# Performance work log

Measured on AMD Instinct MI355X. Metric: run time of the kernel, lower is better.

Reference implementation:

```python
import jax, jax.numpy as jnp
import numpy as np

D_MODEL = 1024
N_HEADS = 16
HEAD_DIM = D_MODEL // N_HEADS


def setup_inputs() -> dict:
    key = jax.random.key(0)
    ks = jax.random.split(key, 6)
    B, S = 2, 2048
    scale = 1.0 / np.sqrt(D_MODEL)
    x = jax.random.normal(ks[0], (B, S, D_MODEL), dtype=jnp.float32)
    Wq = jax.random.normal(ks[1], (D_MODEL, D_MODEL), dtype=jnp.float32) * scale
    Wk = jax.random.normal(ks[2], (D_MODEL, D_MODEL), dtype=jnp.float32) * scale
    Wv = jax.random.normal(ks[3], (D_MODEL, D_MODEL), dtype=jnp.float32) * scale
    Wo = jax.random.normal(ks[4], (D_MODEL, D_MODEL), dtype=jnp.float32) * scale
    bo = jax.random.normal(ks[5], (D_MODEL,), dtype=jnp.float32) * 0.02
    return {"x": x, "Wq": Wq, "Wk": Wk, "Wv": Wv, "Wo": Wo, "bo": bo}


def reference(x, Wq, Wk, Wv, Wo, bo):
    B, S, _ = x.shape
    H, hd = N_HEADS, HEAD_DIM
    # qkv projections (no bias, qkv_bias=False)
    q = (x @ Wq).reshape(B, S, H, hd).transpose(0, 2, 1, 3)  # [B,H,S,hd]
    k = (x @ Wk).reshape(B, S, H, hd).transpose(0, 2, 1, 3)
    v = (x @ Wv).reshape(B, S, H, hd).transpose(0, 2, 1, 3)
    scores = jnp.einsum('bhqd,bhkd->bhqk', q, k)  # [B,H,S,S]
    causal = jnp.tril(jnp.ones((S, S), dtype=bool))  # True = keep
    scores = jnp.where(causal, scores, -jnp.inf)
    weights = jax.nn.softmax(scores / np.sqrt(hd), axis=-1)
    # dropout p=0.0 -> identity
    ctx = jnp.einsum('bhqk,bhkd->bhqd', weights, v)  # [B,H,S,hd]
    ctx = ctx.transpose(0, 2, 1, 3).reshape(B, S, H * hd)
    return ctx @ Wo + bo
```

## Files before the change

kernel.cpp:

```cpp
#include <hip/hip_runtime.h>
#include <hip/hip_bf16.h>
#include <stdint.h>

#define SEQ    2048
#define BATCH  2
#define DMODEL 1024
#define NHEADS 16
#define HDIM   64
#define MROWS  (BATCH*SEQ)

typedef __attribute__((ext_vector_type(8))) short bf16x8;
typedef __attribute__((ext_vector_type(4))) float f32x4;

__device__ inline void global_to_lds16(const void* g, void* l) {
  __builtin_amdgcn_global_load_lds(
      (const __attribute__((address_space(1))) uint32_t*)g,
      (__attribute__((address_space(3))) uint32_t*)l, 16, 0, 0);
}

__device__ inline unsigned short f2bf_bits(float f) {
  __hip_bfloat16 h = __float2bfloat16(f);
  return *(unsigned short*)&h;
}

__global__ void cvt_x(const float* __restrict__ x, __hip_bfloat16* __restrict__ xb) {
  int i = (blockIdx.x * 256 + threadIdx.x) * 4;
  float4 v = *(const float4*)(x + i);
  ushort4 o;
  o.x = f2bf_bits(v.x); o.y = f2bf_bits(v.y);
  o.z = f2bf_bits(v.z); o.w = f2bf_bits(v.w);
  *(ushort4*)(xb + i) = o;
}

__global__ void trans_w(const float* __restrict__ Wq, const float* __restrict__ Wk,
                        const float* __restrict__ Wv, const float* __restrict__ Wo,
                        __hip_bfloat16* __restrict__ Wqkv_t, __hip_bfloat16* __restrict__ Wo_t) {
  __shared__ float tile[32][33];
  int z = blockIdx.z;
  const float* W = (z == 0) ? Wq : (z == 1) ? Wk : (z == 2) ? Wv : Wo;
  __hip_bfloat16* dst = (z < 3) ? (Wqkv_t + (size_t)z * 1024 * 1024) : Wo_t;
  int k0 = blockIdx.x * 32, n0 = blockIdx.y * 32;
  int tx = threadIdx.x & 31, ty = threadIdx.x >> 5;
#pragma unroll
  for (int r = 0; r < 4; r++)
    tile[ty + r * 8][tx] = W[(size_t)(k0 + ty + r * 8) * 1024 + n0 + tx];
  __syncthreads();
#pragma unroll
  for (int r = 0; r < 4; r++)
    dst[(size_t)(n0 + ty + r * 8) * 1024 + k0 + tx] = __float2bfloat16(tile[tx][ty + r * 8]);
}

__global__ void trans_v(const __hip_bfloat16* __restrict__ QKV, __hip_bfloat16* __restrict__ Vt) {
  __shared__ __hip_bfloat16 tile[64][72];
  int bh = blockIdx.y;
  int b = bh >> 4, h = bh & 15;
  int s0 = blockIdx.x * 64;
  int t = threadIdx.x;
  int r = t >> 2, cg = (t & 3) * 16;
  const __hip_bfloat16* src = QKV + ((size_t)(b * SEQ + s0 + r)) * 3072 + 2048 + h * 64 + cg;
  *(uint4*)&tile[r][cg]     = *(const uint4*)src;
  *(uint4*)&tile[r][cg + 8] = *(const uint4*)(src + 8);
  __syncthreads();
  unsigned short tmp[16];
#pragma unroll
  for (int i = 0; i < 16; i++) tmp[i] = *(const unsigned short*)&tile[cg + i][r];
  __hip_bfloat16* dst = Vt + ((size_t)bh * 64 + r) * 2048 + s0 + cg;
  *(uint4*)dst       = *(const uint4*)&tmp[0];
  *(uint4*)(dst + 8) = *(const uint4*)&tmp[8];
}

template <bool OUT_BF16>
__global__ __launch_bounds__(256, 2)
void gemm_kernel(const __hip_bfloat16* __restrict__ A, const __hip_bfloat16* __restrict__ Bt,
                 void* __restrict__ C, const float* __restrict__ bias, int ldc) {
  __shared__ __hip_bfloat16 Asl[128 * 32];
  __shared__ __hip_bfloat16 Bsl[128 * 32];

  const int t = threadIdx.x;
  const int lane = t & 63;
  const int w = t >> 6;
  const int wm = w >> 1, wn = w & 1;
  const int m0 = blockIdx.y * 128;
  const int n0 = blockIdx.x * 128;

  f32x4 acc[4][4];
#pragma unroll
  for (int i = 0; i < 4; i++)
#pragma unroll
    for (int j = 0; j < 4; j++) acc[i][j] = (f32x4){0.f, 0.f, 0.f, 0.f};

  const int rA0 = w * 16 + (lane >> 2);
  const int kof = (lane & 3) * 8;
  const int fm = lane & 15;
  const int fk = (lane >> 4) * 8;

  for (int k0 = 0; k0 < 1024; k0 += 32) {
#pragma unroll
    for (int i = 0; i < 2; i++) {
      int r = rA0 + i * 64;
      global_to_lds16(A + (size_t)(m0 + r) * 1024 + k0 + kof, (void*)(Asl + r * 32 + kof));
      global_to_lds16(Bt + (size_t)(n0 + r) * 1024 + k0 + kof, (void*)(Bsl + r * 32 + kof));
    }
    __syncthreads();
    bf16x8 af[4], bfr[4];
#pragma unroll
    for (int mi = 0; mi < 4; mi++)
      af[mi] = *(const bf16x8*)(Asl + (wm * 64 + mi * 16 + fm) * 32 + fk);
#pragma unroll
    for (int ni = 0; ni < 4; ni++)
      bfr[ni] = *(const bf16x8*)(Bsl + (wn * 64 + ni * 16 + fm) * 32 + fk);
#pragma unroll
    for (int mi = 0; mi < 4; mi++)
#pragma unroll
      for (int ni = 0; ni < 4; ni++)
        acc[mi][ni] = __builtin_amdgcn_mfma_f32_16x16x32_bf16(af[mi], bfr[ni], acc[mi][ni], 0, 0, 0);
    __syncthreads();
  }

#pragma unroll
  for (int mi = 0; mi < 4; mi++) {
    int mb = m0 + wm * 64 + mi * 16 + (lane >> 4) * 4;
#pragma unroll
    for (int ni = 0; ni < 4; ni++) {
      int n = n0 + wn * 64 + ni * 16 + fm;
      float bv = OUT_BF16 ? 0.f : bias[n];
#pragma unroll
      for (int r = 0; r < 4; r++) {
        if (OUT_BF16)
          ((__hip_bfloat16*)C)[(size_t)(mb + r) * ldc + n] = __float2bfloat16(acc[mi][ni][r]);
        else
          ((float*)C)[(size_t)(mb + r) * ldc + n] = acc[mi][ni][r] + bv;
      }
    }
  }
}

__global__ __launch_bounds__(256, 2)
void attn_kernel(const __hip_bfloat16* __restrict__ QKV,
                 const __hip_bfloat16* __restrict__ Vt,
                 __hip_bfloat16* __restrict__ ctx) {
  __shared__ __hip_bfloat16 Klds[64 * 64];
  __shared__ __hip_bfloat16 Vlds[64 * 64];
  __shared__ __hip_bfloat16 Plds[2][64 * 72];

  const int t = threadIdx.x;
  const int lane = t & 63;
  const int w = t >> 6;
  const int jb = blockIdx.x;
  const int qtab[2] = { jb, 31 - jb };
  const int bh = blockIdx.y;
  const int b = bh >> 4, h = bh & 15;
  const int fm = lane & 15;
  const int g4 = lane >> 4;
  const int fk = g4 * 8;
  const size_t rowb = (size_t)b * SEQ;
  const float c = 0.18033688011112042f;

  const int rr = lane >> 3;
  const int jc = (lane & 7) ^ rr;

  bf16x8 qf[2][2];
#pragma unroll
  for (int hh = 0; hh < 2; hh++) {
    const __hip_bfloat16* qp = QKV + (rowb + qtab[hh] * 64 + w * 16 + fm) * 3072 + h * 64 + fk;
    bf16x8 r0 = *(const bf16x8*)qp;
    bf16x8 r1 = *(const bf16x8*)(qp + 32);
#pragma unroll
    for (int i = 0; i < 8; i++) {
      float f0 = __uint_as_float(((unsigned)(unsigned short)r0[i]) << 16) * c;
      float f1 = __uint_as_float(((unsigned)(unsigned short)r1[i]) << 16) * c;
      r0[i] = (short)f2bf_bits(f0);
      r1[i] = (short)f2bf_bits(f1);
    }
    qf[hh][0] = r0; qf[hh][1] = r1;
  }

  bf16x8 ones;
#pragma unroll
  for (int i = 0; i < 8; i++) ones[i] = (short)0x3F80;

  f32x4 acc[2][4];
  f32x4 lacc[2];
#pragma unroll
  for (int hh = 0; hh < 2; hh++) {
    lacc[hh] = (f32x4){0.f, 0.f, 0.f, 0.f};
#pragma unroll
    for (int d = 0; d < 4; d++) acc[hh][d] = (f32x4){0.f, 0.f, 0.f, 0.f};
  }

  for (int ktt = 0; ktt <= qtab[1]; ++ktt) {
    const int kt0 = ktt * 64;
    __syncthreads();
#pragma unroll
    for (int i = 0; i < 2; i++) {
      int seg = w + i * 4;
      int r = seg * 8 + rr;
      global_to_lds16(QKV + (rowb + kt0 + r) * 3072 + 1024 + h * 64 + jc * 8,
                      (void*)(Klds + seg * 512 + lane * 8));
      global_to_lds16(Vt + ((size_t)bh * 64 + r) * 2048 + kt0 + jc * 8,
                      (void*)(Vlds + seg * 512 + lane * 8));
    }
    __syncthreads();

#pragma unroll
    for (int hh = 0; hh < 2; hh++) {
      if (ktt > qtab[hh]) continue;
      f32x4 s[4];
#pragma unroll
      for (int ns = 0; ns < 4; ns++) s[ns] = (f32x4){0.f, 0.f, 0.f, 0.f};
#pragma unroll
      for (int kk = 0; kk < 2; kk++) {
#pragma unroll
        for (int ns = 0; ns < 4; ns++) {
          bf16x8 kf = *(const bf16x8*)(Klds + (ns * 16 + fm) * 64 + (((kk * 4 + g4) ^ (fm & 7)) << 3));
          s[ns] = __builtin_amdgcn_mfma_f32_16x16x32_bf16(qf[hh][kk], kf, s[ns], 0, 0, 0);
        }
      }
      const bool diag = (ktt == qtab[hh]);
      __hip_bfloat16* P = (__hip_bfloat16*)Plds[hh];
#pragma unroll
      for (int ns = 0; ns < 4; ns++)
#pragma unroll
        for (int r = 0; r < 4; r++) {
          bool msk = diag && (ns * 16 + fm > w * 16 + g4 * 4 + r);
          float p = msk ? 0.f : exp2f(s[ns][r]);
          P[(w * 16 + g4 * 4 + r) * 72 + ns * 16 + fm] = __float2bfloat16(p);
        }
#pragma unroll
      for (int kk = 0; kk < 2; kk++) {
        bf16x8 pa = *(const bf16x8*)(P + (w * 16 + fm) * 72 + kk * 32 + fk);
        lacc[hh] = __builtin_amdgcn_mfma_f32_16x16x32_bf16(pa, ones, lacc[hh], 0, 0, 0);
#pragma unroll
        for (int dd = 0; dd < 4; dd++) {
          bf16x8 vf = *(const bf16x8*)(Vlds + (dd * 16 + fm) * 64 + (((kk * 4 + g4) ^ (fm & 7)) << 3));
          acc[hh][dd] = __builtin_amdgcn_mfma_f32_16x16x32_bf16(pa, vf, acc[hh][dd], 0, 0, 0);
        }
      }
    }
  }

#pragma unroll
  for (int hh = 0; hh < 2; hh++) {
#pragma unroll
    for (int dd = 0; dd < 4; dd++)
#pragma unroll
      for (int r = 0; r < 4; r++) {
        int q = qtab[hh] * 64 + w * 16 + g4 * 4 + r;
        ctx[(rowb + q) * 1024 + h * 64 + dd * 16 + fm] =
            __float2bfloat16(acc[hh][dd][r] / lacc[hh][r]);
      }
  }
}

extern "C" void kernel_launch(void* const* d_in, const int* in_sizes, int n_in,
                              void* d_out, int out_size, void* d_ws, size_t ws_size,
                              hipStream_t stream) {
  const float* x  = (const float*)d_in[0];
  const float* Wq = (const float*)d_in[1];
  const float* Wk = (const float*)d_in[2];
  const float* Wv = (const float*)d_in[3];
  const float* Wo = (const float*)d_in[4];
  const float* bo = (const float*)d_in[5];
  float* out = (float*)d_out;

  char* ws = (char*)d_ws;
  __hip_bfloat16* xb     = (__hip_bfloat16*)(ws);
  __hip_bfloat16* Wqkv_t = (__hip_bfloat16*)(ws + (8ull  << 20));
  __hip_bfloat16* Wo_t   = (__hip_bfloat16*)(ws + (14ull << 20));
  __hip_bfloat16* QKV    = (__hip_bfloat16*)(ws + (16ull << 20));
  __hip_bfloat16* ctxb   = (__hip_bfloat16*)(ws + (40ull << 20));
  __hip_bfloat16* Vt     = xb;

  cvt_x<<<dim3(MROWS * DMODEL / (256 * 4)), dim3(256), 0, stream>>>(x, xb);
  trans_w<<<dim3(32, 32, 4), dim3(256), 0, stream>>>(Wq, Wk, Wv, Wo, Wqkv_t, Wo_t);
  gemm_kernel<true><<<dim3(24, 32), dim3(256), 0, stream>>>(xb, Wqkv_t, (void*)QKV, nullptr, 3072);
  trans_v<<<dim3(32, 32), dim3(256), 0, stream>>>(QKV, Vt);
  attn_kernel<<<dim3(16, 32), dim3(256), 0, stream>>>(QKV, Vt, ctxb);
  gemm_kernel<false><<<dim3(8, 32), dim3(256), 0, stream>>>(ctxb, Wo_t, (void*)out, bo, 1024);
}
```

Measured before the change: 199.3 us.

## Stage 128-key K/V tiles in attention and retile output GEMM to 128x64

The attention kernel now loads 128 keys of K and V per barrier pair instead of 64, and processes them as two 64-wide sub-chunks. This halves the number of synchronisation and load rounds, at the cost of double the K/V LDS footprint. The V layout uses a new 16-slot XOR swizzle. The output projection GEMM switches to 128x64 tiles with each wave owning 32 rows, which doubles the grid to fill more CUs. The QKV GEMM's launch bounds now ask for 3 workgroups per CU, which may constrain registers.

```diff
diff --git a/kernel.cpp b/kernel.cpp
--- a/kernel.cpp
+++ b/kernel.cpp
@@ -69,23 +69,25 @@
   *(uint4*)(dst + 8) = *(const uint4*)&tmp[8];
 }
 
-template <bool OUT_BF16>
-__global__ __launch_bounds__(256, 2)
+template <int TN, bool OUT_BF16, int MINW>
+__global__ __launch_bounds__(256, MINW)
 void gemm_kernel(const __hip_bfloat16* __restrict__ A, const __hip_bfloat16* __restrict__ Bt,
                  void* __restrict__ C, const float* __restrict__ bias, int ldc) {
   __shared__ __hip_bfloat16 Asl[128 * 32];
-  __shared__ __hip_bfloat16 Bsl[128 * 32];
+  __shared__ __hip_bfloat16 Bsl[TN * 32];
 
   const int t = threadIdx.x;
   const int lane = t & 63;
   const int w = t >> 6;
-  const int wm = w >> 1, wn = w & 1;
+  constexpr int MI = (TN == 128) ? 4 : 2;
+  const int wrow = (TN == 128) ? (w >> 1) * 64 : w * 32;
+  const int wcol = (TN == 128) ? (w & 1) * 64 : 0;
   const int m0 = blockIdx.y * 128;
-  const int n0 = blockIdx.x * 128;
-
-  f32x4 acc[4][4];
-#pragma unroll
-  for (int i = 0; i < 4; i++)
+  const int n0 = blockIdx.x * TN;
+
+  f32x4 acc[MI][4];
+#pragma unroll
+  for (int i = 0; i < MI; i++)
 #pragma unroll
     for (int j = 0; j < 4; j++) acc[i][j] = (f32x4){0.f, 0.f, 0.f, 0.f};
 
@@ -99,18 +101,22 @@
     for (int i = 0; i < 2; i++) {
       int r = rA0 + i * 64;
       global_to_lds16(A + (size_t)(m0 + r) * 1024 + k0 + kof, (void*)(Asl + r * 32 + kof));
+    }
+#pragma unroll
+    for (int i = 0; i < TN / 64; i++) {
+      int r = rA0 + i * 64;
       global_to_lds16(Bt + (size_t)(n0 + r) * 1024 + k0 + kof, (void*)(Bsl + r * 32 + kof));
     }
     __syncthreads();
-    bf16x8 af[4], bfr[4];
-#pragma unroll
-    for (int mi = 0; mi < 4; mi++)
-      af[mi] = *(const bf16x8*)(Asl + (wm * 64 + mi * 16 + fm) * 32 + fk);
+    bf16x8 af[MI], bfr[4];
+#pragma unroll
+    for (int mi = 0; mi < MI; mi++)
+      af[mi] = *(const bf16x8*)(Asl + (wrow + mi * 16 + fm) * 32 + fk);
 #pragma unroll
     for (int ni = 0; ni < 4; ni++)
-      bfr[ni] = *(const bf16x8*)(Bsl + (wn * 64 + ni * 16 + fm) * 32 + fk);
-#pragma unroll
-    for (int mi = 0; mi < 4; mi++)
+      bfr[ni] = *(const bf16x8*)(Bsl + (wcol + ni * 16 + fm) * 32 + fk);
+#pragma unroll
+    for (int mi = 0; mi < MI; mi++)
 #pragma unroll
       for (int ni = 0; ni < 4; ni++)
         acc[mi][ni] = __builtin_amdgcn_mfma_f32_16x16x32_bf16(af[mi], bfr[ni], acc[mi][ni], 0, 0, 0);
@@ -118,11 +124,11 @@
   }
 
 #pragma unroll
-  for (int mi = 0; mi < 4; mi++) {
-    int mb = m0 + wm * 64 + mi * 16 + (lane >> 4) * 4;
+  for (int mi = 0; mi < MI; mi++) {
+    int mb = m0 + wrow + mi * 16 + (lane >> 4) * 4;
 #pragma unroll
     for (int ni = 0; ni < 4; ni++) {
-      int n = n0 + wn * 64 + ni * 16 + fm;
+      int n = n0 + wcol + ni * 16 + fm;
       float bv = OUT_BF16 ? 0.f : bias[n];
 #pragma unroll
       for (int r = 0; r < 4; r++) {
@@ -139,8 +145,8 @@
 void attn_kernel(const __hip_bfloat16* __restrict__ QKV,
                  const __hip_bfloat16* __restrict__ Vt,
                  __hip_bfloat16* __restrict__ ctx) {
-  __shared__ __hip_bfloat16 Klds[64 * 64];
-  __shared__ __hip_bfloat16 Vlds[64 * 64];
+  __shared__ __hip_bfloat16 Klds[128 * 64];
+  __shared__ __hip_bfloat16 Vlds[64 * 128];
   __shared__ __hip_bfloat16 Plds[2][64 * 72];
 
   const int t = threadIdx.x;
@@ -156,8 +162,10 @@
   const size_t rowb = (size_t)b * SEQ;
   const float c = 0.18033688011112042f;
 
-  const int rr = lane >> 3;
-  const int jc = (lane & 7) ^ rr;
+  const int krr = lane >> 3;
+  const int kjc = (lane & 7) ^ krr;
+  const int vrr = lane >> 4;
+  const int vjc = (lane & 15) ^ vrr;
 
   bf16x8 qf[2][2];
 #pragma unroll
@@ -188,52 +196,60 @@
     for (int d = 0; d < 4; d++) acc[hh][d] = (f32x4){0.f, 0.f, 0.f, 0.f};
   }
 
-  for (int ktt = 0; ktt <= qtab[1]; ++ktt) {
-    const int kt0 = ktt * 64;
-    __syncthreads();
-#pragma unroll
-    for (int i = 0; i < 2; i++) {
+  const int lastt = qtab[1] >> 1;
+  for (int ktt2 = 0; ktt2 <= lastt; ++ktt2) {
+    const int kt0 = ktt2 * 128;
+    __syncthreads();
+#pragma unroll
+    for (int i = 0; i < 4; i++) {
       int seg = w + i * 4;
-      int r = seg * 8 + rr;
-      global_to_lds16(QKV + (rowb + kt0 + r) * 3072 + 1024 + h * 64 + jc * 8,
+      int kr = seg * 8 + krr;
+      global_to_lds16(QKV + (rowb + kt0 + kr) * 3072 + 1024 + h * 64 + kjc * 8,
                       (void*)(Klds + seg * 512 + lane * 8));
-      global_to_lds16(Vt + ((size_t)bh * 64 + r) * 2048 + kt0 + jc * 8,
+      int vr = seg * 4 + vrr;
+      global_to_lds16(Vt + ((size_t)bh * 64 + vr) * 2048 + kt0 + vjc * 8,
                       (void*)(Vlds + seg * 512 + lane * 8));
     }
     __syncthreads();
 
 #pragma unroll
-    for (int hh = 0; hh < 2; hh++) {
-      if (ktt > qtab[hh]) continue;
-      f32x4 s[4];
-#pragma unroll
-      for (int ns = 0; ns < 4; ns++) s[ns] = (f32x4){0.f, 0.f, 0.f, 0.f};
-#pragma unroll
-      for (int kk = 0; kk < 2; kk++) {
-#pragma unroll
-        for (int ns = 0; ns < 4; ns++) {
-          bf16x8 kf = *(const bf16x8*)(Klds + (ns * 16 + fm) * 64 + (((kk * 4 + g4) ^ (fm & 7)) << 3));
-          s[ns] = __builtin_amdgcn_mfma_f32_16x16x32_bf16(qf[hh][kk], kf, s[ns], 0, 0, 0);
+    for (int sc = 0; sc < 2; sc++) {
+      const int kts = ktt2 * 2 + sc;
+#pragma unroll
+      for (int hh = 0; hh < 2; hh++) {
+        if (kts > qtab[hh]) continue;
+        f32x4 s[4];
+#pragma unroll
+        for (int ns = 0; ns < 4; ns++) s[ns] = (f32x4){0.f, 0.f, 0.f, 0.f};
+#pragma unroll
+        for (int kk = 0; kk < 2; kk++) {
+#pragma unroll
+          for (int ns = 0; ns < 4; ns++) {
+            int row = sc * 64 + ns * 16 + fm;
+            bf16x8 kf = *(const bf16x8*)(Klds + row * 64 + (((kk * 4 + g4) ^ (fm & 7)) << 3));
+            s[ns] = __builtin_amdgcn_mfma_f32_16x16x32_bf16(qf[hh][kk], kf, s[ns], 0, 0, 0);
+          }
         }
-      }
-      const bool diag = (ktt == qtab[hh]);
-      __hip_bfloat16* P = (__hip_bfloat16*)Plds[hh];
-#pragma unroll
-      for (int ns = 0; ns < 4; ns++)
-#pragma unroll
-        for (int r = 0; r < 4; r++) {
-          bool msk = diag && (ns * 16 + fm > w * 16 + g4 * 4 + r);
-          float p = msk ? 0.f : exp2f(s[ns][r]);
-          P[(w * 16 + g4 * 4 + r) * 72 + ns * 16 + fm] = __float2bfloat16(p);
-        }
-#pragma unroll
-      for (int kk = 0; kk < 2; kk++) {
-        bf16x8 pa = *(const bf16x8*)(P + (w * 16 + fm) * 72 + kk * 32 + fk);
-        lacc[hh] = __builtin_amdgcn_mfma_f32_16x16x32_bf16(pa, ones, lacc[hh], 0, 0, 0);
-#pragma unroll
-        for (int dd = 0; dd < 4; dd++) {
-          bf16x8 vf = *(const bf16x8*)(Vlds + (dd * 16 + fm) * 64 + (((kk * 4 + g4) ^ (fm & 7)) << 3));
-          acc[hh][dd] = __builtin_amdgcn_mfma_f32_16x16x32_bf16(pa, vf, acc[hh][dd], 0, 0, 0);
+        const bool diag = (kts == qtab[hh]);
+        __hip_bfloat16* P = (__hip_bfloat16*)Plds[hh];
+#pragma unroll
+        for (int ns = 0; ns < 4; ns++)
+#pragma unroll
+          for (int r = 0; r < 4; r++) {
+            bool msk = diag && (ns * 16 + fm > w * 16 + g4 * 4 + r);
+            float p = msk ? 0.f : exp2f(s[ns][r]);
+            P[(w * 16 + g4 * 4 + r) * 72 + ns * 16 + fm] = __float2bfloat16(p);
+          }
+#pragma unroll
+        for (int kk = 0; kk < 2; kk++) {
+          bf16x8 pa = *(const bf16x8*)(P + (w * 16 + fm) * 72 + kk * 32 + fk);
+          lacc[hh] = __builtin_amdgcn_mfma_f32_16x16x32_bf16(pa, ones, lacc[hh], 0, 0, 0);
+#pragma unroll
+          for (int dd = 0; dd < 4; dd++) {
+            int vslot = (sc * 8 + kk * 4 + g4) ^ (fm & 3);
+            bf16x8 vf = *(const bf16x8*)(Vlds + (dd * 16 + fm) * 128 + vslot * 8);
+            acc[hh][dd] = __builtin_amdgcn_mfma_f32_16x16x32_bf16(pa, vf, acc[hh][dd], 0, 0, 0);
+          }
         }
       }
     }
@@ -273,8 +289,8 @@
 
   cvt_x<<<dim3(MROWS * DMODEL / (256 * 4)), dim3(256), 0, stream>>>(x, xb);
   trans_w<<<dim3(32, 32, 4), dim3(256), 0, stream>>>(Wq, Wk, Wv, Wo, Wqkv_t, Wo_t);
-  gemm_kernel<true><<<dim3(24, 32), dim3(256), 0, stream>>>(xb, Wqkv_t, (void*)QKV, nullptr, 3072);
+  gemm_kernel<128, true, 3><<<dim3(24, 32), dim3(256), 0, stream>>>(xb, Wqkv_t, (void*)QKV, nullptr, 3072);
   trans_v<<<dim3(32, 32), dim3(256), 0, stream>>>(QKV, Vt);
   attn_kernel<<<dim3(16, 32), dim3(256), 0, stream>>>(QKV, Vt, ctxb);
-  gemm_kernel<false><<<dim3(8, 32), dim3(256), 0, stream>>>(ctxb, Wo_t, (void*)out, bo, 1024);
-}
+  gemm_kernel<64, false, 2><<<dim3(16, 32), dim3(256), 0, stream>>>(ctxb, Wo_t, (void*)out, bo, 1024);
+}
```

After: 196.0 us. No clear change (-1.6%).
